# Kernel tuning notes

Measured on AMD Instinct MI355X. Metric: run time of the kernel, lower is better.

The kernel has to match this reference:

```python
import jax, jax.numpy as jnp
import numpy as np


def conv1d(x, w, b):
    # x: (N, Cin, W), w: (Cout, Cin, K) -> (N, Cout, W-K+1), VALID conv (torch Conv1d)
    y = jax.lax.conv_general_dilated(x, w, (1,), 'VALID', dimension_numbers=('NCH', 'OIH', 'NCH'))
    return y + b[None, :, None]


def cnn_block(x, w, b):
    # conv1d then MaxPool1d over the full valid length -> (N, Cout)
    return jnp.max(conv1d(x, w, b), axis=2)


def highway(x, Wp, bp, Wg, bg):
    p = jax.nn.relu(x @ Wp.T + bp)
    g = jax.nn.sigmoid(x @ Wg.T + bg)
    return g * p + (1.0 - g) * x


def lstm_masked(x, lens, Wih, Whh, bih, bhh):
    # x: (N, Wt, E); lens: (N,) valid lengths. Emulates pack_padded_sequence +
    # nn.LSTM + pad_packed_sequence: outputs are h_t for t < len, zeros after.
    N, Wt, _ = x.shape
    H = Whh.shape[1]
    bias = bih + bhh
    h0 = jnp.zeros((N, H), x.dtype)

    def step(carry, inp):
        xt, t = inp
        h, c = carry
        z = xt @ Wih.T + h @ Whh.T + bias  # (N, 4H), gate order i,f,g,o
        i, f, g, o = jnp.split(z, 4, axis=-1)
        c2 = jax.nn.sigmoid(f) * c + jax.nn.sigmoid(i) * jnp.tanh(g)
        h2 = jax.nn.sigmoid(o) * jnp.tanh(c2)
        valid = (t < lens)[:, None]
        h2 = jnp.where(valid, h2, h)
        c2 = jnp.where(valid, c2, c)
        return (h2, c2), jnp.where(valid, h2, jnp.zeros_like(h2))

    xs = jnp.moveaxis(x, 1, 0)  # (Wt, N, E)
    ts = jnp.arange(Wt)
    _, out = jax.lax.scan(step, (h0, h0), (xs, ts))
    return jnp.moveaxis(out, 0, 1)  # (N, Wt, H)


def setup_inputs() -> dict:
    key = jax.random.key(0)
    ks = jax.random.split(key, 32)
    B, T = 32, 48
    WL, WA, WE = 33, 50, 30
    EL, EA, EE, H = 300, 988, 20, 128
    CL, CA, CE = 128, 256, 64
    s = 0.02
    inp = {
        'x_lin': jax.random.normal(ks[0], (B, T, WL, EL), jnp.float32),
        'x_aco': jax.random.normal(ks[1], (B, T, WA, EA), jnp.float32),
        'x_emo': jax.random.normal(ks[2], (B, T, WE, EE), jnp.float32),
        'window_length': jax.random.randint(ks[3], (B, T), 0, WE).astype(jnp.int32) + 1,
        'length': jax.random.randint(ks[4], (B,), 1, T + 1).astype(jnp.int32),
        # CNN params
        'convL_w': s * jax.random.normal(ks[5], (CL, EL, 5), jnp.float32),
        'convL_b': jnp.zeros((CL,), jnp.float32),
        'convA_w': s * jax.random.normal(ks[6], (CA, EA, 10), jnp.float32),
        'convA_b': jnp.zeros((CA,), jnp.float32),
        'convE_w': s * jax.random.normal(ks[7], (CE, H, 3), jnp.float32),
        'convE_b': jnp.zeros((CE,), jnp.float32),
        # Highway params
        'hwL_Wp': s * jax.random.normal(ks[8], (CL, CL), jnp.float32),
        'hwL_bp': jnp.zeros((CL,), jnp.float32),
        'hwL_Wg': s * jax.random.normal(ks[9], (CL, CL), jnp.float32),
        'hwL_bg': jnp.zeros((CL,), jnp.float32),
        'hwA_Wp': s * jax.random.normal(ks[10], (CA, CA), jnp.float32),
        'hwA_bp': jnp.zeros((CA,), jnp.float32),
        'hwA_Wg': s * jax.random.normal(ks[11], (CA, CA), jnp.float32),
        'hwA_bg': jnp.zeros((CA,), jnp.float32),
        'hwE_Wp': s * jax.random.normal(ks[12], (CE, CE), jnp.float32),
        'hwE_bp': jnp.zeros((CE,), jnp.float32),
        'hwE_Wg': s * jax.random.normal(ks[13], (CE, CE), jnp.float32),
        'hwE_bg': jnp.zeros((CE,), jnp.float32),
        # LSTM params (nn.LSTM, 1 layer, batch_first)
        'lstm_Wih': s * jax.random.normal(ks[14], (4 * H, EE), jnp.float32),
        'lstm_Whh': s * jax.random.normal(ks[15], (4 * H, H), jnp.float32),
        'lstm_bih': jnp.zeros((4 * H,), jnp.float32),
        'lstm_bhh': jnp.zeros((4 * H,), jnp.float32),
    }
    return inp


def reference(x_lin, x_aco, x_emo, window_length, length,
              convL_w, convL_b, convA_w, convA_b, convE_w, convE_b,
              hwL_Wp, hwL_bp, hwL_Wg, hwL_bg,
              hwA_Wp, hwA_bp, hwA_Wg, hwA_bg,
              hwE_Wp, hwE_bp, hwE_Wg, hwE_bg,
              lstm_Wih, lstm_Whh, lstm_bih, lstm_bhh):
    B, T = x_lin.shape[:2]
    # Linguistic: per-window CNN + Highway (dropout = identity in eval)
    xl = x_lin.reshape(B * T, x_lin.shape[2], x_lin.shape[3]).transpose(0, 2, 1)  # (BT, 300, WL)
    outL = highway(cnn_block(xl, convL_w, convL_b), hwL_Wp, hwL_bp, hwL_Wg, hwL_bg)
    outL = outL.reshape(B, T, -1)
    # Acoustic
    xa = x_aco.reshape(B * T, x_aco.shape[2], x_aco.shape[3]).transpose(0, 2, 1)  # (BT, 988, WA)
    outA = highway(cnn_block(xa, convA_w, convA_b), hwA_Wp, hwA_bp, hwA_Wg, hwA_bg)
    outA = outA.reshape(B, T, -1)
    # Emotient: ragged per-window LSTM (packed semantics) -> CNN -> Highway
    xe = x_emo.reshape(B * T, x_emo.shape[2], x_emo.shape[3])  # (BT, WE, 20)
    lens = window_length.reshape(B * T)
    h = lstm_masked(xe, lens, lstm_Wih, lstm_Whh, lstm_bih, lstm_bhh)  # (BT, WE, 128)
    outE = highway(cnn_block(h.transpose(0, 2, 1), convE_w, convE_b), hwE_Wp, hwE_bp, hwE_Wg, hwE_bg)
    outE = outE.reshape(B, T, -1)
    # Concatenate modalities -> (B, T, 128+256+64) fed to the downstream head
    return jnp.concatenate([outL, outA, outE], axis=2)
```

## Files before the change

kernel.cpp:

```cpp
#include <hip/hip_runtime.h>
#include <hip/hip_bf16.h>
#include <math.h>

#define BTOT 1536
#define EL 300
#define ELP 304
#define WL_ 33
#define CL 128
#define LOUTL 29
#define KPL 1536
#define EA 988
#define EAP 992
#define WA_ 50
#define CA 256
#define LOUTA 41
#define KPA 9920
#define EE 20
#define WE_ 30
#define HH 128
#define CE 64
#define LOUTE 28
#define KPE 384
#define KDIML 1500
#define KDIMA 9880
#define KDIME 384

typedef __attribute__((ext_vector_type(4))) float f32x4;
typedef __attribute__((ext_vector_type(8))) short short8;

__device__ __forceinline__ unsigned short f2bf(float f) {
    unsigned int x = __float_as_uint(f);
    unsigned int r = (x + 0x7fffu + ((x >> 16) & 1u)) >> 16;
    return (unsigned short)r;
}

__device__ __forceinline__ float sigmf(float x) {
    return __builtin_amdgcn_rcpf(1.f + __expf(-x));
}
__device__ __forceinline__ float tanh_fast(float x) {
    return 1.f - 2.f * __builtin_amdgcn_rcpf(1.f + __expf(2.f * x));
}

#define GLD16(gp, lp) __builtin_amdgcn_global_load_lds( \
    (const __attribute__((address_space(1))) void*)(gp), \
    (__attribute__((address_space(3))) void*)(lp), 16, 0, 0)

template<int N> __device__ __forceinline__ void vmwait() {
    if constexpr (N == 0) asm volatile("s_waitcnt vmcnt(0)" ::: "memory");
    else if constexpr (N == 3) asm volatile("s_waitcnt vmcnt(3)" ::: "memory");
    else if constexpr (N == 4) asm volatile("s_waitcnt vmcnt(4)" ::: "memory");
    else if constexpr (N == 6) asm volatile("s_waitcnt vmcnt(6)" ::: "memory");
    else static_assert(N == 0 || N == 3 || N == 4 || N == 6, "add case");
}

__device__ __forceinline__ void tr_one(const float* a, float* at, int R, int C, int idx) {
    int r = idx / C, c = idx - r * C;
    at[c * R + r] = a[idx];
}
template<int CIN, int CINP, int KW, int COUT, int KPAD>
__device__ __forceinline__ void wt_one(const float* w, unsigned short* wt, int idx) {
    int co = idx / KPAD;
    int p  = idx - co * KPAD;
    int k  = p / CINP;
    int c  = p - k * CINP;
    float v = 0.f;
    if (k < KW && c < CIN) v = w[(co * CIN + c) * KW + k];
    wt[idx] = f2bf(v);
}
template<bool BIG>
__global__ void prep_small(const float* hwL_Wp, float* WpTL, const float* hwL_Wg, float* WgTL,
                           const float* hwA_Wp, float* WpTA, const float* hwA_Wg, float* WgTA,
                           const float* hwE_Wp, float* WpTE, const float* hwE_Wg, float* WgTE,
                           const float* lstm_Wih, float* WihT, const float* lstm_Whh, float* WhhT,
                           const float* convL_w, unsigned short* wtL,
                           const float* convE_w, unsigned short* wtE,
                           unsigned short* whh_bf, unsigned short* wihp_bf) {
    constexpr int S1 = 16384, S2 = 16384, S3 = 65536, S4 = 65536, S5 = 4096, S6 = 4096;
    constexpr int S7 = 512 * 20, S8 = 512 * 128;
    constexpr int S9 = 128 * KPL, S10 = 64 * KPE, S11 = 512 * 128, S12 = 512 * 32;
    constexpr int SMALL = S1 + S2 + S3 + S4 + S5 + S6 + S7 + S8;
    constexpr int TOTAL = BIG ? (SMALL + S9 + S10 + S11 + S12) : SMALL;
    int stride = gridDim.x * blockDim.x;
    for (int i = blockIdx.x * blockDim.x + threadIdx.x; i < TOTAL; i += stride) {
        int idx = i;
        if (idx < S1) { tr_one(hwL_Wp, WpTL, 128, 128, idx); continue; } idx -= S1;
        if (idx < S2) { tr_one(hwL_Wg, WgTL, 128, 128, idx); continue; } idx -= S2;
        if (idx < S3) { tr_one(hwA_Wp, WpTA, 256, 256, idx); continue; } idx -= S3;
        if (idx < S4) { tr_one(hwA_Wg, WgTA, 256, 256, idx); continue; } idx -= S4;
        if (idx < S5) { tr_one(hwE_Wp, WpTE, 64, 64, idx); continue; } idx -= S5;
        if (idx < S6) { tr_one(hwE_Wg, WgTE, 64, 64, idx); continue; } idx -= S6;
        if (idx < S7) { tr_one(lstm_Wih, WihT, 512, 20, idx); continue; } idx -= S7;
        if (idx < S8) { tr_one(lstm_Whh, WhhT, 512, 128, idx); continue; } idx -= S8;
        if constexpr (BIG) {
            if (idx < S9) { wt_one<EL, ELP, 5, CL, KPL>(convL_w, wtL, idx); continue; } idx -= S9;
            if (idx < S10) { wt_one<HH, HH, 3, CE, KPE>(convE_w, wtE, idx); continue; } idx -= S10;
            if (idx < S11) { whh_bf[idx] = f2bf(lstm_Whh[idx]); continue; } idx -= S11;
            { int col = idx >> 5, e = idx & 31;
              wihp_bf[idx] = (e < 20) ? f2bf(lstm_Wih[col * 20 + e]) : (unsigned short)0; }
        }
    }
}

__global__ void prep_wtA(const float* __restrict__ w, unsigned short* __restrict__ wt) {
    int idx = blockIdx.x * blockDim.x + threadIdx.x;
    if (idx >= CA * KPA) return;
    wt_one<EA, EAP, 10, CA, KPA>(w, wt, idx);
}

template<int CIN, int CINP>
__device__ __forceinline__ void cvt_chunk(const float* in, unsigned short* out, int idx) {
    constexpr int CH = CINP / 8;
    int row = idx / CH, c0 = (idx - row * CH) * 8;
    const float* src = in + (size_t)row * CIN + c0;
    union { short8 s; unsigned short u[8]; } o;
    if (c0 + 8 <= CIN) {
        float4 v0 = *(const float4*)src;
        float4 v1 = *(const float4*)(src + 4);
        o.u[0]=f2bf(v0.x); o.u[1]=f2bf(v0.y); o.u[2]=f2bf(v0.z); o.u[3]=f2bf(v0.w);
        o.u[4]=f2bf(v1.x); o.u[5]=f2bf(v1.y); o.u[6]=f2bf(v1.z); o.u[7]=f2bf(v1.w);
    } else {
        #pragma unroll
        for (int j = 0; j < 8; ++j) o.u[j] = (c0 + j < CIN) ? f2bf(src[j]) : (unsigned short)0;
    }
    *(short8*)(out + (size_t)row * CINP + c0) = o.s;
}
__global__ void cvt_both(const float* __restrict__ xa, const float* __restrict__ xl,
                         unsigned short* __restrict__ outa, unsigned short* __restrict__ outl) {
    constexpr int NAC = (BTOT * WA_) * (EAP / 8);
    constexpr int NLC = (BTOT * WL_) * (ELP / 8);
    int stride = gridDim.x * blockDim.x;
    for (int i = blockIdx.x * blockDim.x + threadIdx.x; i < NAC + NLC; i += stride) {
        if (i < NAC) cvt_chunk<EA, EAP>(xa, outa, i);
        else         cvt_chunk<EL, ELP>(xl, outl, i - NAC);
    }
}

template<int NBT, int LOUT, int WIN, int CINP, int COUT, int KPAD, int BM, int BN, int NS>
__global__ __launch_bounds__(256, 2)
void conv_pool_v6(const unsigned short* __restrict__ xb, const unsigned short* __restrict__ wt,
                  const float* __restrict__ bias, float* __restrict__ pooled)
{
    constexpr int MFR  = BM / 32;
    constexpr int NFR  = BN / 32;
    constexpr int A_IT = BM / 64;
    constexpr int B_IT = BN / 64;
    constexpr int VMN  = A_IT + B_IT;
    constexpr int ABY  = BM * 64;
    constexpr int BUFB = (BM + BN) * 64;
    constexpr int NK   = KPAD / 32;
    constexpr int MVAL = NBT * LOUT;
    constexpr int MT   = BTOT / NBT;
    constexpr int EPI  = BM * 36 * 4;
    constexpr int SMSZ = (3 * BUFB > EPI) ? 3 * BUFB : EPI;

    __shared__ __align__(16) char smem[SMSZ];

    const int tid  = threadIdx.x;
    const int lane = tid & 63;
    const int wid  = tid >> 6;
    const int wm   = wid >> 1;
    const int wn   = wid & 1;
    const int lr   = lane & 15;
    const int lq   = lane >> 4;

    int m, n;
    if constexpr (NS == 2) {
        int xcd = blockIdx.x & 7;
        n = xcd & 1;
        m = (xcd >> 1) * (MT / 4) + (blockIdx.x >> 3);
    } else {
        m = blockIdx.x; n = 0;
    }

    f32x4 acc[MFR][NFR];
    #pragma unroll
    for (int i = 0; i < MFR; ++i)
        #pragma unroll
        for (int j = 0; j < NFR; ++j) acc[i][j] = (f32x4){0.f, 0.f, 0.f, 0.f};

    const char* asrc[A_IT];
    #pragma unroll
    for (int i = 0; i < A_IT; ++i) {
        int c = tid + i * 256;
        int r = c >> 2, slot = c & 3;
        int rv = (r < MVAL) ? r : (MVAL - 1);
        int btl = rv / LOUT, l = rv - btl * LOUT;
        asrc[i] = (const char*)xb + (((size_t)(m * NBT + btl) * WIN + l) * CINP) * 2
                + ((slot * 16) ^ (((r >> 1) & 3) << 4));
    }
    const char* bsrc[B_IT];
    #pragma unroll
    for (int i = 0; i < B_IT; ++i) {
        int c = tid + i * 256;
        int col = c >> 2, slot = c & 3;
        bsrc[i] = (const char*)wt + ((size_t)(n * BN + col) * KPAD) * 2
                + ((slot * 16) ^ (((col >> 1) & 3) << 4));
    }

    auto STAGE = [&](int ts, int buf) {
        char* db = smem + buf * BUFB;
        #pragma unroll
        for (int i = 0; i < A_IT; ++i)
            GLD16(asrc[i] + (size_t)ts * 64, db + i * 4096 + wid * 1024);
        #pragma unroll
        for (int i = 0; i < B_IT; ++i)
            GLD16(bsrc[i] + (size_t)ts * 64, db + ABY + i * 4096 + wid * 1024);
    };

    STAGE(0, 0);
    STAGE(1, 1);
    vmwait<VMN>();
    __builtin_amdgcn_s_barrier();

    const int rbase = wm * (BM / 2) + lr;
    const int cbase = wn * (BN / 2) + lr;
    int cur = 0;
    for (int t = 0; t < NK; ++t) {
        const char* sA = smem + cur * BUFB;
        const char* sB = sA + ABY;
        short8 a[MFR];
        #pragma unroll
        for (int o = 0; o < MFR; ++o) {
            int r = rbase + o * 16;
            a[o] = *(const short8*)(sA + (size_t)r * 64 + ((lq * 16) ^ (((r >> 1) & 3) << 4)));
        }
        short8 bfr[NFR];
        #pragma unroll
        for (int nf = 0; nf < NFR; ++nf) {
            int cb = cbase + nf * 16;
            bfr[nf] = *(const short8*)(sB + (size_t)cb * 64 + ((lq * 16) ^ (((cb >> 1) & 3) << 4)));
        }
        int wb = cur + 2; if (wb >= 3) wb -= 3;
        if (t + 2 < NK) STAGE(t + 2, wb);
        asm volatile("s_waitcnt lgkmcnt(0)" ::: "memory");
        __builtin_amdgcn_sched_barrier(0);
        __builtin_amdgcn_s_setprio(1);
        #pragma unroll
        for (int nf = 0; nf < NFR; ++nf)
            #pragma unroll
            for (int o = 0; o < MFR; ++o)
                acc[o][nf] = __builtin_amdgcn_mfma_f32_16x16x32_bf16(a[o], bfr[nf], acc[o][nf], 0, 0, 0);
        __builtin_amdgcn_s_setprio(0);
        if (t + 2 < NK) vmwait<VMN>(); else vmwait<0>();
        asm volatile("" ::: "memory");
        __builtin_amdgcn_s_barrier();
        cur = cur + 1; if (cur >= 3) cur -= 3;
    }
    __syncthreads();

    float* smf = (float*)smem;
    for (int nf = 0; nf < NFR; ++nf) {
        #pragma unroll
        for (int o = 0; o < MFR; ++o) {
            int row = wm * (BM / 2) + o * 16 + lq * 4;
            int cs  = wn * 16 + lr;
            f32x4 v = acc[o][nf];
            #pragma unroll
            for (int r = 0; r < 4; ++r)
                smf[(size_t)(row + r) * 36 + cs] = v[r];
        }
        __syncthreads();
        if (tid < 32 * NBT) {
            int btl = tid >> 5, cs = tid & 31;
            int base = btl * LOUT;
            float mx = smf[(size_t)base * 36 + cs];
            for (int l = 1; l < LOUT; ++l)
                mx = fmaxf(mx, smf[(size_t)(base + l) * 36 + cs]);
            int col = n * BN + (cs >> 4) * (BN / 2) + nf * 16 + (cs & 15);
            int bt  = m * NBT + btl;
            pooled[(size_t)bt * COUT + col] = mx + bias[col];
        }
        __syncthreads();
    }
}

__global__ __launch_bounds__(512, 1)
void lstm_mfma(const float* __restrict__ x_emo,
               const unsigned short* __restrict__ wihp_bf, const unsigned short* __restrict__ whh_bf,
               const float* __restrict__ bih, const float* __restrict__ bhh,
               const int* __restrict__ lens, unsigned short* __restrict__ hbuf)
{
    __shared__ __align__(16) unsigned short xq[WE_ * 16 * 32];
    __shared__ __align__(16) char h_s[2 * 16 * HH * 2];

    const int tid  = threadIdx.x;
    const int w    = tid >> 6;
    const int lane = tid & 63;
    const int lr   = lane & 15;
    const int lq   = lane >> 4;
    const int s0   = blockIdx.x * 16;
    const int c    = w * 16 + lr;

    short8 bfr[4][4];
    short8 bw[4];
    float bj[4];
    #pragma unroll
    for (int g = 0; g < 4; ++g) {
        int col = g * 128 + c;
        #pragma unroll
        for (int kt = 0; kt < 4; ++kt)
            bfr[g][kt] = *(const short8*)(whh_bf + (size_t)col * 128 + kt * 32 + lq * 8);
        bw[g] = *(const short8*)(wihp_bf + (size_t)col * 32 + lq * 8);
        bj[g] = bih[col] + bhh[col];
    }
    int len4[4];
    #pragma unroll
    for (int j = 0; j < 4; ++j) len4[j] = lens[s0 + lq * 4 + j];

    for (int i = tid; i < WE_ * 16 * 32; i += 512) {
        int t = i >> 9, r = (i >> 5) & 15, e = i & 31;
        xq[i] = (e < 20) ? f2bf(x_emo[(((size_t)(s0 + r) * WE_) + t) * 20 + e]) : (unsigned short)0;
    }
    for (int i = tid; i < 2048; i += 512) ((unsigned int*)h_s)[i] = 0u;

    float c_prev[4] = {0.f, 0.f, 0.f, 0.f};
    unsigned short hb_prev[4] = {0, 0, 0, 0};
    __syncthreads();

    for (int t = 0; t < WE_; ++t) {
        const char* hsr = h_s + (t & 1) * 4096;
        char* hsw = h_s + ((t & 1) ^ 1) * 4096;
        short8 ax = *(const short8*)((const char*)xq + (size_t)(t * 16 + lr) * 64 + lq * 16);
        short8 af[4];
        #pragma unroll
        for (int kt = 0; kt < 4; ++kt)
            af[kt] = *(const short8*)(hsr + ((lr * 256 + kt * 64 + lq * 16) ^ ((lr & 7) << 4)));
        f32x4 acc[4];
        #pragma unroll
        for (int g = 0; g < 4; ++g)
            acc[g] = __builtin_amdgcn_mfma_f32_16x16x32_bf16(ax, bw[g], (f32x4){0.f,0.f,0.f,0.f}, 0, 0, 0);
        #pragma unroll
        for (int kt = 0; kt < 4; ++kt)
            #pragma unroll
            for (int g = 0; g < 4; ++g)
                acc[g] = __builtin_amdgcn_mfma_f32_16x16x32_bf16(af[kt], bfr[g][kt], acc[g], 0, 0, 0);
        #pragma unroll
        for (int j = 0; j < 4; ++j) {
            int s = lq * 4 + j;
            float zi = acc[0][j] + bj[0];
            float zf = acc[1][j] + bj[1];
            float zg = acc[2][j] + bj[2];
            float zo = acc[3][j] + bj[3];
            float si = sigmf(zi), sf = sigmf(zf), so = sigmf(zo);
            float tg = tanh_fast(zg);
            float c2 = sf * c_prev[j] + si * tg;
            float h2 = so * tanh_fast(c2);
            bool valid = (t < len4[j]);
            c_prev[j] = valid ? c2 : c_prev[j];
            unsigned short h2b = f2bf(h2);
            unsigned short hn = valid ? h2b : hb_prev[j];
            hb_prev[j] = hn;
            *(unsigned short*)(hsw + (((s * HH + c) * 2) ^ ((s & 7) << 4))) = hn;
            hbuf[(((size_t)(s0 + s) * WE_) + t) * HH + c] = valid ? h2b : (unsigned short)0;
        }
        __syncthreads();
    }
}

__global__ __launch_bounds__(256)
void highway_all(const float* __restrict__ pL, const float* __restrict__ pA, const float* __restrict__ pE,
                 const float* __restrict__ WpTL, const float* __restrict__ bpL,
                 const float* __restrict__ WgTL, const float* __restrict__ bgL,
                 const float* __restrict__ WpTA, const float* __restrict__ bpA,
                 const float* __restrict__ WgTA, const float* __restrict__ bgA,
                 const float* __restrict__ WpTE, const float* __restrict__ bpE,
                 const float* __restrict__ WgTE, const float* __restrict__ bgE,
                 float* __restrict__ out) {
    __shared__ float xs[256];
    int bx = blockIdx.x;
    int tid = threadIdx.x;
    if (bx < BTOT) {
        xs[tid] = pA[(size_t)bx * 256 + tid];
        __syncthreads();
        float ap = bpA[tid], ag = bgA[tid];
        for (int c = 0; c < 256; ++c) {
            float xv = xs[c];
            ap += xv * WpTA[c * 256 + tid];
            ag += xv * WgTA[c * 256 + tid];
        }
        float pp = fmaxf(ap, 0.f);
        float g = sigmf(ag);
        out[(size_t)bx * 448 + 128 + tid] = g * pp + (1.f - g) * xs[tid];
    } else {
        int bt = bx - BTOT;
        if (tid < 128) xs[tid] = pL[(size_t)bt * 128 + tid];
        else if (tid < 192) xs[64 + tid] = pE[(size_t)bt * 64 + (tid - 128)];
        __syncthreads();
        if (tid < 128) {
            float ap = bpL[tid], ag = bgL[tid];
            for (int c = 0; c < 128; ++c) {
                float xv = xs[c];
                ap += xv * WpTL[c * 128 + tid];
                ag += xv * WgTL[c * 128 + tid];
            }
            float pp = fmaxf(ap, 0.f);
            float g = sigmf(ag);
            out[(size_t)bt * 448 + tid] = g * pp + (1.f - g) * xs[tid];
        } else if (tid < 192) {
            int j = tid - 128;
            float ap = bpE[j], ag = bgE[j];
            for (int c = 0; c < 64; ++c) {
                float xv = xs[192 + c];
                ap += xv * WpTE[c * 64 + j];
                ag += xv * WgTE[c * 64 + j];
            }
            float pp = fmaxf(ap, 0.f);
            float g = sigmf(ag);
            out[(size_t)bt * 448 + 384 + j] = g * pp + (1.f - g) * xs[192 + j];
        }
    }
}

__global__ __launch_bounds__(512)
void lstm_kernel_f32(const float* __restrict__ x, const int* __restrict__ lens,
                     const float* __restrict__ WihT, const float* __restrict__ WhhT,
                     const float* __restrict__ bih, const float* __restrict__ bhh,
                     float* __restrict__ hout) {
    int bt = blockIdx.x;
    int j  = threadIdx.x;
    __shared__ float xs[WE_][EE];
    __shared__ __align__(16) float hs[HH];
    __shared__ float zs[512];
    for (int idx = j; idx < WE_ * EE; idx += 512)
        ((float*)xs)[idx] = x[(size_t)bt * WE_ * EE + idx];
    if (j < HH) hs[j] = 0.f;
    float wih[EE];
    #pragma unroll
    for (int e = 0; e < EE; ++e) wih[e] = WihT[e * 512 + j];
    float whh[HH];
    #pragma unroll
    for (int h = 0; h < HH; ++h) whh[h] = WhhT[h * 512 + j];
    float bjv = bih[j] + bhh[j];
    float c_reg = 0.f;
    int len = lens[bt];
    __syncthreads();
    for (int t = 0; t < WE_; ++t) {
        float z = bjv;
        #pragma unroll
        for (int e = 0; e < EE; ++e) z += wih[e] * xs[t][e];
        const float4* h4 = (const float4*)hs;
        #pragma unroll
        for (int q = 0; q < HH / 4; ++q) {
            float4 hv = h4[q];
            z += whh[4*q+0] * hv.x + whh[4*q+1] * hv.y
               + whh[4*q+2] * hv.z + whh[4*q+3] * hv.w;
        }
        zs[j] = z;
        __syncthreads();
        if (j < HH) {
            float zi = zs[j], zf = zs[HH + j], zg = zs[2*HH + j], zo = zs[3*HH + j];
            float si = 1.f / (1.f + expf(-zi));
            float sf = 1.f / (1.f + expf(-zf));
            float so = 1.f / (1.f + expf(-zo));
            float tg = tanhf(zg);
            float c2 = sf * c_reg + si * tg;
            float h2 = so * tanhf(c2);
            bool valid = (t < len);
            float hn = valid ? h2 : hs[j];
            c_reg    = valid ? c2 : c_reg;
            hout[((size_t)bt * WE_ + t) * HH + j] = valid ? h2 : 0.f;
            hs[j] = hn;
        }
        __syncthreads();
    }
}

template<int CIN, int WIN, int COUT, int KDIM, int LOUT>
__global__ __launch_bounds__(256)
void conv_pool_simple(const float* __restrict__ x, const float* __restrict__ w,
                      const float* __restrict__ bias, float* __restrict__ pooled)
{
    constexpr int KW = KDIM / CIN;
    int bt = blockIdx.x;
    int co = blockIdx.y * 64 + (threadIdx.x & 63);
    int seg = threadIdx.x >> 6;
    __shared__ float part[4][64];
    float m = -INFINITY;
    for (int l = seg; l < LOUT; l += 4) {
        float acc = 0.f;
        for (int k = 0; k < KW; ++k) {
            const float* xr = x + ((size_t)bt * WIN + l + k) * CIN;
            const float* wr = w + ((size_t)co * CIN) * KW + k;
            for (int cc = 0; cc < CIN; ++cc) acc += xr[cc] * wr[(size_t)cc * KW];
        }
        m = fmaxf(m, acc);
    }
    part[seg][threadIdx.x & 63] = m;
    __syncthreads();
    if (threadIdx.x < 64) {
        float mm = fmaxf(fmaxf(part[0][threadIdx.x], part[1][threadIdx.x]),
                         fmaxf(part[2][threadIdx.x], part[3][threadIdx.x]));
        pooled[(size_t)bt * COUT + co] = mm + bias[co];
    }
}

static inline int cdiv(int a, int b) { return (a + b - 1) / b; }

extern "C" void kernel_launch(void* const* d_in, const int* in_sizes, int n_in,
                              void* d_out, int out_size, void* d_ws, size_t ws_size,
                              hipStream_t stream) {
    const float* x_lin  = (const float*)d_in[0];
    const float* x_aco  = (const float*)d_in[1];
    const float* x_emo  = (const float*)d_in[2];
    const int*   wlen   = (const int*)  d_in[3];
    const float* convL_w = (const float*)d_in[5];
    const float* convL_b = (const float*)d_in[6];
    const float* convA_w = (const float*)d_in[7];
    const float* convA_b = (const float*)d_in[8];
    const float* convE_w = (const float*)d_in[9];
    const float* convE_b = (const float*)d_in[10];
    const float* hwL_Wp = (const float*)d_in[11];
    const float* hwL_bp = (const float*)d_in[12];
    const float* hwL_Wg = (const float*)d_in[13];
    const float* hwL_bg = (const float*)d_in[14];
    const float* hwA_Wp = (const float*)d_in[15];
    const float* hwA_bp = (const float*)d_in[16];
    const float* hwA_Wg = (const float*)d_in[17];
    const float* hwA_bg = (const float*)d_in[18];
    const float* hwE_Wp = (const float*)d_in[19];
    const float* hwE_bp = (const float*)d_in[20];
    const float* hwE_Wg = (const float*)d_in[21];
    const float* hwE_bg = (const float*)d_in[22];
    const float* lstm_Wih = (const float*)d_in[23];
    const float* lstm_Whh = (const float*)d_in[24];
    const float* lstm_bih = (const float*)d_in[25];
    const float* lstm_bhh = (const float*)d_in[26];
    float* out = (float*)d_out;

    char* p0 = (char*)d_ws;
    char* p = p0;
    auto alloc = [&](size_t bytes) { char* r = p; p += (bytes + 255) & ~(size_t)255; return r; };
    float* WpTL = (float*)alloc((size_t)CL * CL * 4);
    float* WgTL = (float*)alloc((size_t)CL * CL * 4);
    float* WpTA = (float*)alloc((size_t)CA * CA * 4);
    float* WgTA = (float*)alloc((size_t)CA * CA * 4);
    float* WpTE = (float*)alloc((size_t)CE * CE * 4);
    float* WgTE = (float*)alloc((size_t)CE * CE * 4);
    float* WihT = (float*)alloc((size_t)EE * 512 * 4);
    float* WhhT = (float*)alloc((size_t)HH * 512 * 4);
    unsigned short* whh_bf  = (unsigned short*)alloc((size_t)512 * 128 * 2);
    unsigned short* wihp_bf = (unsigned short*)alloc((size_t)512 * 32 * 2);
    void*  hbuf = (void*)alloc((size_t)BTOT * WE_ * HH * 4);
    float* pL   = (float*)alloc((size_t)BTOT * CL * 4);
    float* pA   = (float*)alloc((size_t)BTOT * CA * 4);
    float* pE   = (float*)alloc((size_t)BTOT * CE * 4);
    unsigned short* wtA = (unsigned short*)alloc((size_t)CA * KPA * 2);
    unsigned short* wtL = (unsigned short*)alloc((size_t)CL * KPL * 2);
    unsigned short* wtE = (unsigned short*)alloc((size_t)CE * KPE * 2);
    unsigned short* xlin_p = (unsigned short*)alloc((size_t)BTOT * WL_ * ELP * 2 + 64);
    unsigned short* xaco_p = (unsigned short*)alloc((size_t)BTOT * WA_ * EAP * 2 + 64);
    size_t need = (size_t)(p - p0);
    bool big = ws_size >= need;

    if (big) {
        prep_small<true><<<2048, 256, 0, stream>>>(hwL_Wp, WpTL, hwL_Wg, WgTL, hwA_Wp, WpTA, hwA_Wg, WgTA,
                                                   hwE_Wp, WpTE, hwE_Wg, WgTE, lstm_Wih, WihT, lstm_Whh, WhhT,
                                                   convL_w, wtL, convE_w, wtE, whh_bf, wihp_bf);
        prep_wtA<<<cdiv(CA * KPA, 256), 256, 0, stream>>>(convA_w, wtA);
        lstm_mfma<<<BTOT / 16, 512, 0, stream>>>(x_emo, wihp_bf, whh_bf, lstm_bih, lstm_bhh, wlen,
                                                 (unsigned short*)hbuf);
        cvt_both<<<4096, 256, 0, stream>>>(x_aco, x_lin, xaco_p, xlin_p);
        conv_pool_v6<6, LOUTA, WA_, EAP, CA, KPA, 256, 128, 2>
            <<<512, 256, 0, stream>>>(xaco_p, wtA, convA_b, pA);
        conv_pool_v6<4, LOUTL, WL_, ELP, CL, KPL, 128, 128, 1>
            <<<BTOT / 4, 256, 0, stream>>>(xlin_p, wtL, convL_b, pL);
        conv_pool_v6<4, LOUTE, WE_, HH, CE, KPE, 128, 64, 1>
            <<<BTOT / 4, 256, 0, stream>>>((const unsigned short*)hbuf, wtE, convE_b, pE);
    } else {
        prep_small<false><<<2048, 256, 0, stream>>>(hwL_Wp, WpTL, hwL_Wg, WgTL, hwA_Wp, WpTA, hwA_Wg, WgTA,
                                                    hwE_Wp, WpTE, hwE_Wg, WgTE, lstm_Wih, WihT, lstm_Whh, WhhT,
                                                    convL_w, wtL, convE_w, wtE, whh_bf, wihp_bf);
        lstm_kernel_f32<<<BTOT, 512, 0, stream>>>(x_emo, wlen, WihT, WhhT, lstm_bih, lstm_bhh, (float*)hbuf);
        conv_pool_simple<EA, WA_, CA, KDIMA, LOUTA>
            <<<dim3(BTOT, CA / 64), 256, 0, stream>>>(x_aco, convA_w, convA_b, pA);
        conv_pool_simple<EL, WL_, CL, KDIML, LOUTL>
            <<<dim3(BTOT, CL / 64), 256, 0, stream>>>(x_lin, convL_w, convL_b, pL);
        conv_pool_simple<HH, WE_, CE, KDIME, LOUTE>
            <<<dim3(BTOT, CE / 64), 256, 0, stream>>>((const float*)hbuf, convE_w, convE_b, pE);
    }

    highway_all<<<2 * BTOT, 256, 0, stream>>>(pL, pA, pE,
                                              WpTL, hwL_bp, WgTL, hwL_bg,
                                              WpTA, hwA_bp, WgTA, hwA_bg,
                                              WpTE, hwE_bp, WgTE, hwE_bg, out);
}
```

Baseline: 627.4 us.

## Rewrite conv-pool as shifted-window implicit GEMM and fuse prep/cvt launches

Replaces the im2col-style conv_pool_v6 with conv_pool_v8, which loads each input window chunk once into LDS and reuses it across all kernel taps by shifting rows. It also pools in registers with lane shuffles instead of an LDS epilogue. The weight layout changes to per-tap channel blocks, so ELP is padded to 320 for 32-aligned chunks. The conv A weight prep moves into the shared prep kernel, and the input bf16 conversion runs as extra blocks of the LSTM kernel, cutting launches and overlapping the conversion with the serial LSTM. This adds wasted padded K work for the linguistic path and uses hand-tuned vmcnt waits that must match the issue order exactly.

```diff
diff --git a/kernel.cpp b/kernel.cpp
--- a/kernel.cpp
+++ b/kernel.cpp
@@ -4,11 +4,11 @@
 
 #define BTOT 1536
 #define EL 300
-#define ELP 304
+#define ELP 320
 #define WL_ 33
 #define CL 128
 #define LOUTL 29
-#define KPL 1536
+#define KPL 1600
 #define EA 988
 #define EAP 992
 #define WA_ 50
@@ -47,10 +47,13 @@
 
 template<int N> __device__ __forceinline__ void vmwait() {
     if constexpr (N == 0) asm volatile("s_waitcnt vmcnt(0)" ::: "memory");
-    else if constexpr (N == 3) asm volatile("s_waitcnt vmcnt(3)" ::: "memory");
+    else if constexpr (N == 1) asm volatile("s_waitcnt vmcnt(1)" ::: "memory");
+    else if constexpr (N == 2) asm volatile("s_waitcnt vmcnt(2)" ::: "memory");
     else if constexpr (N == 4) asm volatile("s_waitcnt vmcnt(4)" ::: "memory");
+    else if constexpr (N == 5) asm volatile("s_waitcnt vmcnt(5)" ::: "memory");
     else if constexpr (N == 6) asm volatile("s_waitcnt vmcnt(6)" ::: "memory");
-    else static_assert(N == 0 || N == 3 || N == 4 || N == 6, "add case");
+    else if constexpr (N == 8) asm volatile("s_waitcnt vmcnt(8)" ::: "memory");
+    else static_assert(N == 0, "add case");
 }
 
 __device__ __forceinline__ void tr_one(const float* a, float* at, int R, int C, int idx) {
@@ -68,18 +71,20 @@
     wt[idx] = f2bf(v);
 }
 template<bool BIG>
-__global__ void prep_small(const float* hwL_Wp, float* WpTL, const float* hwL_Wg, float* WgTL,
-                           const float* hwA_Wp, float* WpTA, const float* hwA_Wg, float* WgTA,
-                           const float* hwE_Wp, float* WpTE, const float* hwE_Wg, float* WgTE,
-                           const float* lstm_Wih, float* WihT, const float* lstm_Whh, float* WhhT,
-                           const float* convL_w, unsigned short* wtL,
-                           const float* convE_w, unsigned short* wtE,
-                           unsigned short* whh_bf, unsigned short* wihp_bf) {
+__global__ void prep_all(const float* hwL_Wp, float* WpTL, const float* hwL_Wg, float* WgTL,
+                         const float* hwA_Wp, float* WpTA, const float* hwA_Wg, float* WgTA,
+                         const float* hwE_Wp, float* WpTE, const float* hwE_Wg, float* WgTE,
+                         const float* lstm_Wih, float* WihT, const float* lstm_Whh, float* WhhT,
+                         const float* convL_w, unsigned short* wtL,
+                         const float* convE_w, unsigned short* wtE,
+                         const float* convA_w, unsigned short* wtA,
+                         unsigned short* whh_bf, unsigned short* wihp_bf) {
     constexpr int S1 = 16384, S2 = 16384, S3 = 65536, S4 = 65536, S5 = 4096, S6 = 4096;
     constexpr int S7 = 512 * 20, S8 = 512 * 128;
     constexpr int S9 = 128 * KPL, S10 = 64 * KPE, S11 = 512 * 128, S12 = 512 * 32;
+    constexpr int S13 = CA * KPA;
     constexpr int SMALL = S1 + S2 + S3 + S4 + S5 + S6 + S7 + S8;
-    constexpr int TOTAL = BIG ? (SMALL + S9 + S10 + S11 + S12) : SMALL;
+    constexpr int TOTAL = BIG ? (SMALL + S9 + S10 + S11 + S12 + S13) : SMALL;
     int stride = gridDim.x * blockDim.x;
     for (int i = blockIdx.x * blockDim.x + threadIdx.x; i < TOTAL; i += stride) {
         int idx = i;
@@ -95,16 +100,12 @@
             if (idx < S9) { wt_one<EL, ELP, 5, CL, KPL>(convL_w, wtL, idx); continue; } idx -= S9;
             if (idx < S10) { wt_one<HH, HH, 3, CE, KPE>(convE_w, wtE, idx); continue; } idx -= S10;
             if (idx < S11) { whh_bf[idx] = f2bf(lstm_Whh[idx]); continue; } idx -= S11;
-            { int col = idx >> 5, e = idx & 31;
-              wihp_bf[idx] = (e < 20) ? f2bf(lstm_Wih[col * 20 + e]) : (unsigned short)0; }
-        }
-    }
-}
-
-__global__ void prep_wtA(const float* __restrict__ w, unsigned short* __restrict__ wt) {
-    int idx = blockIdx.x * blockDim.x + threadIdx.x;
-    if (idx >= CA * KPA) return;
-    wt_one<EA, EAP, 10, CA, KPA>(w, wt, idx);
+            if (idx < S12) { int col = idx >> 5, e = idx & 31;
+                             wihp_bf[idx] = (e < 20) ? f2bf(lstm_Wih[col * 20 + e]) : (unsigned short)0;
+                             continue; } idx -= S12;
+            wt_one<EA, EAP, 10, CA, KPA>(convA_w, wtA, idx);
+        }
+    }
 }
 
 template<int CIN, int CINP>
@@ -124,164 +125,31 @@
     }
     *(short8*)(out + (size_t)row * CINP + c0) = o.s;
 }
-__global__ void cvt_both(const float* __restrict__ xa, const float* __restrict__ xl,
-                         unsigned short* __restrict__ outa, unsigned short* __restrict__ outl) {
-    constexpr int NAC = (BTOT * WA_) * (EAP / 8);
-    constexpr int NLC = (BTOT * WL_) * (ELP / 8);
-    int stride = gridDim.x * blockDim.x;
-    for (int i = blockIdx.x * blockDim.x + threadIdx.x; i < NAC + NLC; i += stride) {
-        if (i < NAC) cvt_chunk<EA, EAP>(xa, outa, i);
-        else         cvt_chunk<EL, ELP>(xl, outl, i - NAC);
-    }
-}
-
-template<int NBT, int LOUT, int WIN, int CINP, int COUT, int KPAD, int BM, int BN, int NS>
-__global__ __launch_bounds__(256, 2)
-void conv_pool_v6(const unsigned short* __restrict__ xb, const unsigned short* __restrict__ wt,
-                  const float* __restrict__ bias, float* __restrict__ pooled)
-{
-    constexpr int MFR  = BM / 32;
-    constexpr int NFR  = BN / 32;
-    constexpr int A_IT = BM / 64;
-    constexpr int B_IT = BN / 64;
-    constexpr int VMN  = A_IT + B_IT;
-    constexpr int ABY  = BM * 64;
-    constexpr int BUFB = (BM + BN) * 64;
-    constexpr int NK   = KPAD / 32;
-    constexpr int MVAL = NBT * LOUT;
-    constexpr int MT   = BTOT / NBT;
-    constexpr int EPI  = BM * 36 * 4;
-    constexpr int SMSZ = (3 * BUFB > EPI) ? 3 * BUFB : EPI;
-
-    __shared__ __align__(16) char smem[SMSZ];
-
-    const int tid  = threadIdx.x;
-    const int lane = tid & 63;
-    const int wid  = tid >> 6;
-    const int wm   = wid >> 1;
-    const int wn   = wid & 1;
-    const int lr   = lane & 15;
-    const int lq   = lane >> 4;
-
-    int m, n;
-    if constexpr (NS == 2) {
-        int xcd = blockIdx.x & 7;
-        n = xcd & 1;
-        m = (xcd >> 1) * (MT / 4) + (blockIdx.x >> 3);
-    } else {
-        m = blockIdx.x; n = 0;
-    }
-
-    f32x4 acc[MFR][NFR];
-    #pragma unroll
-    for (int i = 0; i < MFR; ++i)
-        #pragma unroll
-        for (int j = 0; j < NFR; ++j) acc[i][j] = (f32x4){0.f, 0.f, 0.f, 0.f};
-
-    const char* asrc[A_IT];
-    #pragma unroll
-    for (int i = 0; i < A_IT; ++i) {
-        int c = tid + i * 256;
-        int r = c >> 2, slot = c & 3;
-        int rv = (r < MVAL) ? r : (MVAL - 1);
-        int btl = rv / LOUT, l = rv - btl * LOUT;
-        asrc[i] = (const char*)xb + (((size_t)(m * NBT + btl) * WIN + l) * CINP) * 2
-                + ((slot * 16) ^ (((r >> 1) & 3) << 4));
-    }
-    const char* bsrc[B_IT];
-    #pragma unroll
-    for (int i = 0; i < B_IT; ++i) {
-        int c = tid + i * 256;
-        int col = c >> 2, slot = c & 3;
-        bsrc[i] = (const char*)wt + ((size_t)(n * BN + col) * KPAD) * 2
-                + ((slot * 16) ^ (((col >> 1) & 3) << 4));
-    }
-
-    auto STAGE = [&](int ts, int buf) {
-        char* db = smem + buf * BUFB;
-        #pragma unroll
-        for (int i = 0; i < A_IT; ++i)
-            GLD16(asrc[i] + (size_t)ts * 64, db + i * 4096 + wid * 1024);
-        #pragma unroll
-        for (int i = 0; i < B_IT; ++i)
-            GLD16(bsrc[i] + (size_t)ts * 64, db + ABY + i * 4096 + wid * 1024);
-    };
-
-    STAGE(0, 0);
-    STAGE(1, 1);
-    vmwait<VMN>();
-    __builtin_amdgcn_s_barrier();
-
-    const int rbase = wm * (BM / 2) + lr;
-    const int cbase = wn * (BN / 2) + lr;
-    int cur = 0;
-    for (int t = 0; t < NK; ++t) {
-        const char* sA = smem + cur * BUFB;
-        const char* sB = sA + ABY;
-        short8 a[MFR];
-        #pragma unroll
-        for (int o = 0; o < MFR; ++o) {
-            int r = rbase + o * 16;
-            a[o] = *(const short8*)(sA + (size_t)r * 64 + ((lq * 16) ^ (((r >> 1) & 3) << 4)));
-        }
-        short8 bfr[NFR];
-        #pragma unroll
-        for (int nf = 0; nf < NFR; ++nf) {
-            int cb = cbase + nf * 16;
-            bfr[nf] = *(const short8*)(sB + (size_t)cb * 64 + ((lq * 16) ^ (((cb >> 1) & 3) << 4)));
-        }
-        int wb = cur + 2; if (wb >= 3) wb -= 3;
-        if (t + 2 < NK) STAGE(t + 2, wb);
-        asm volatile("s_waitcnt lgkmcnt(0)" ::: "memory");
-        __builtin_amdgcn_sched_barrier(0);
-        __builtin_amdgcn_s_setprio(1);
-        #pragma unroll
-        for (int nf = 0; nf < NFR; ++nf)
-            #pragma unroll
-            for (int o = 0; o < MFR; ++o)
-                acc[o][nf] = __builtin_amdgcn_mfma_f32_16x16x32_bf16(a[o], bfr[nf], acc[o][nf], 0, 0, 0);
-        __builtin_amdgcn_s_setprio(0);
-        if (t + 2 < NK) vmwait<VMN>(); else vmwait<0>();
-        asm volatile("" ::: "memory");
-        __builtin_amdgcn_s_barrier();
-        cur = cur + 1; if (cur >= 3) cur -= 3;
-    }
-    __syncthreads();
-
-    float* smf = (float*)smem;
-    for (int nf = 0; nf < NFR; ++nf) {
-        #pragma unroll
-        for (int o = 0; o < MFR; ++o) {
-            int row = wm * (BM / 2) + o * 16 + lq * 4;
-            int cs  = wn * 16 + lr;
-            f32x4 v = acc[o][nf];
-            #pragma unroll
-            for (int r = 0; r < 4; ++r)
-                smf[(size_t)(row + r) * 36 + cs] = v[r];
-        }
-        __syncthreads();
-        if (tid < 32 * NBT) {
-            int btl = tid >> 5, cs = tid & 31;
-            int base = btl * LOUT;
-            float mx = smf[(size_t)base * 36 + cs];
-            for (int l = 1; l < LOUT; ++l)
-                mx = fmaxf(mx, smf[(size_t)(base + l) * 36 + cs]);
-            int col = n * BN + (cs >> 4) * (BN / 2) + nf * 16 + (cs & 15);
-            int bt  = m * NBT + btl;
-            pooled[(size_t)bt * COUT + col] = mx + bias[col];
-        }
-        __syncthreads();
-    }
-}
+
+#define LSTM_BLOCKS 96
+#define CVT_BLOCKS 1952
 
 __global__ __launch_bounds__(512, 1)
-void lstm_mfma(const float* __restrict__ x_emo,
-               const unsigned short* __restrict__ wihp_bf, const unsigned short* __restrict__ whh_bf,
-               const float* __restrict__ bih, const float* __restrict__ bhh,
-               const int* __restrict__ lens, unsigned short* __restrict__ hbuf)
+void lstm_cvt(const float* __restrict__ x_emo,
+              const unsigned short* __restrict__ wihp_bf, const unsigned short* __restrict__ whh_bf,
+              const float* __restrict__ bih, const float* __restrict__ bhh,
+              const int* __restrict__ lens, unsigned short* __restrict__ hbuf,
+              const float* __restrict__ xa, const float* __restrict__ xl,
+              unsigned short* __restrict__ outa, unsigned short* __restrict__ outl)
 {
     __shared__ __align__(16) unsigned short xq[WE_ * 16 * 32];
     __shared__ __align__(16) char h_s[2 * 16 * HH * 2];
+
+    if (blockIdx.x >= LSTM_BLOCKS) {
+        constexpr int NAC = (BTOT * WA_) * (EAP / 8);
+        constexpr int NLC = (BTOT * WL_) * (ELP / 8);
+        int stride = CVT_BLOCKS * 512;
+        for (int i = (blockIdx.x - LSTM_BLOCKS) * 512 + threadIdx.x; i < NAC + NLC; i += stride) {
+            if (i < NAC) cvt_chunk<EA, EAP>(xa, outa, i);
+            else         cvt_chunk<EL, ELP>(xl, outl, i - NAC);
+        }
+        return;
+    }
 
     const int tid  = threadIdx.x;
     const int w    = tid >> 6;
@@ -354,6 +222,179 @@
             hbuf[(((size_t)(s0 + s) * WE_) + t) * HH + c] = valid ? h2b : (unsigned short)0;
         }
         __syncthreads();
+    }
+}
+
+template<int LOUT, int WIN, int CINP, int KW, int BN, int NS, int MFR, int COUT>
+__global__ __launch_bounds__(256, 2)
+void conv_pool_v8(const unsigned short* __restrict__ xb, const unsigned short* __restrict__ wt,
+                  const float* __restrict__ bias, float* __restrict__ pooled)
+{
+    constexpr int CCH   = CINP / 32;
+    constexpr int KB    = CINP * 2;
+    constexpr int KTOTB = CINP * KW * 2;
+    constexpr int NFR   = BN / 16;
+    constexpr int B_IT  = BN / 64;
+    constexpr int ABUF  = 4 * 64 * 64;
+    constexpr int BBUF  = BN * 64;
+    constexpr int CPQ   = (BTOT / 4) / 4;
+
+    __shared__ __align__(16) char smem[2 * ABUF + 4 * BBUF];
+
+    const int tid  = threadIdx.x;
+    const int lane = tid & 63;
+    const int wid  = tid >> 6;
+    const int lr   = lane & 15;
+    const int lq   = lane >> 4;
+    const int lq16 = lq * 16;
+
+    int m, n;
+    if constexpr (NS == 2) {
+        int xcd = blockIdx.x & 7;
+        n = xcd & 1;
+        m = (xcd >> 1) * CPQ + (blockIdx.x >> 3);
+    } else {
+        m = blockIdx.x; n = 0;
+    }
+
+    f32x4 acc[MFR][NFR];
+    #pragma unroll
+    for (int i = 0; i < MFR; ++i)
+        #pragma unroll
+        for (int j = 0; j < NFR; ++j) acc[i][j] = (f32x4){0.f, 0.f, 0.f, 0.f};
+
+    const int aw_r = tid >> 2;
+    const int aw   = (aw_r < WIN) ? aw_r : (WIN - 1);
+    const int slot = tid & 3;
+    const char* asrc[4];
+    #pragma unroll
+    for (int i = 0; i < 4; ++i)
+        asrc[i] = (const char*)xb + ((size_t)((m * 4 + i) * WIN + aw)) * KB
+                + ((slot * 16) ^ (((aw_r >> 1) & 3) << 4));
+    const char* bsrc[B_IT];
+    #pragma unroll
+    for (int i = 0; i < B_IT; ++i) {
+        int col = (tid + i * 256) >> 2;
+        bsrc[i] = (const char*)wt + (size_t)(n * BN + col) * KTOTB
+                + ((slot * 16) ^ (((col >> 1) & 3) << 4));
+    }
+
+    char* const abuf0 = smem;
+    char* const abuf1 = smem + ABUF;
+    char* const bbase = smem + 2 * ABUF;
+
+    int cbo[NFR];
+    #pragma unroll
+    for (int nf = 0; nf < NFR; ++nf) {
+        int cb = nf * 16 + lr;
+        cbo[nf] = cb * 64 + (lq16 ^ (((cb >> 1) & 3) << 4));
+    }
+
+    #pragma unroll
+    for (int i = 0; i < 4; ++i)
+        GLD16(asrc[i], abuf0 + i * 4096 + tid * 16);
+    #pragma unroll
+    for (int s = 0; s < 3; ++s)
+        #pragma unroll
+        for (int i = 0; i < B_IT; ++i)
+            GLD16(bsrc[i] + s * KB, bbase + s * BBUF + i * 4096 + tid * 16);
+    vmwait<0>();
+    __builtin_amdgcn_s_barrier();
+
+    int bcur = 0;
+
+#define STEP(KK, WN, TAIL) do {                                                    \
+    const char* bb = bbase + bcur * BBUF;                                          \
+    short8 afr[MFR];                                                               \
+    _Pragma("unroll")                                                              \
+    for (int o = 0; o < MFR; ++o) {                                                \
+        int row = o * 16 + lr + (KK);                                              \
+        afr[o] = *(const short8*)(awave + row * 64 + (lq16 ^ (((row >> 1) & 3) << 4))); \
+    }                                                                              \
+    short8 bf[NFR];                                                                \
+    _Pragma("unroll")                                                              \
+    for (int nf = 0; nf < NFR; ++nf) bf[nf] = *(const short8*)(bb + cbo[nf]);      \
+    if (!(TAIL) || (KK) < KW - 3) {                                                \
+        constexpr int k3_ = ((KK) + 3 < KW) ? (KK) + 3 : (KK) + 3 - KW;            \
+        int boff = k3_ * KB + (((KK) + 3 < KW) ? ci : ci + 1) * 64;                \
+        char* bstg = bbase + ((bcur + 3) & 3) * BBUF;                              \
+        _Pragma("unroll")                                                          \
+        for (int i = 0; i < B_IT; ++i)                                             \
+            GLD16(bsrc[i] + boff, bstg + i * 4096 + tid * 16);                     \
+    }                                                                              \
+    if (!(TAIL)) {                                                                 \
+        if (KW >= 8) {                                                             \
+            if ((KK) < 4)                                                          \
+                GLD16(asrc[(KK) & 3] + (size_t)(ci + 1) * 64, abn + ((KK) & 3) * 4096 + tid * 16); \
+        } else if ((KK) == 0) {                                                    \
+            _Pragma("unroll")                                                      \
+            for (int i = 0; i < 4; ++i)                                            \
+                GLD16(asrc[i] + (size_t)(ci + 1) * 64, abn + i * 4096 + tid * 16); \
+        }                                                                          \
+    }                                                                              \
+    asm volatile("s_waitcnt lgkmcnt(0)" ::: "memory");                             \
+    __builtin_amdgcn_sched_barrier(0);                                             \
+    __builtin_amdgcn_s_setprio(1);                                                 \
+    _Pragma("unroll")                                                              \
+    for (int nf = 0; nf < NFR; ++nf)                                               \
+        _Pragma("unroll")                                                          \
+        for (int o = 0; o < MFR; ++o)                                              \
+            acc[o][nf] = __builtin_amdgcn_mfma_f32_16x16x32_bf16(afr[o], bf[nf], acc[o][nf], 0, 0, 0); \
+    __builtin_amdgcn_s_setprio(0);                                                 \
+    vmwait<WN>();                                                                  \
+    asm volatile("" ::: "memory");                                                 \
+    __builtin_amdgcn_s_barrier();                                                  \
+    bcur = (bcur + 1) & 3;                                                         \
+} while (0)
+
+    for (int ci = 0; ci < CCH - 1; ++ci) {
+        const char* ab = (ci & 1) ? abuf1 : abuf0;
+        char* abn = (ci & 1) ? abuf0 : abuf1;
+        const char* awave = ab + wid * 4096;
+        if constexpr (KW == 10) {
+            STEP(0, 5, false); STEP(1, 6, false); STEP(2, 6, false); STEP(3, 6, false);
+            STEP(4, 5, false); STEP(5, 4, false); STEP(6, 4, false); STEP(7, 4, false);
+            STEP(8, 4, false); STEP(9, 4, false);
+        } else if constexpr (KW == 5) {
+            STEP(0, 8, false); STEP(1, 8, false); STEP(2, 4, false); STEP(3, 4, false); STEP(4, 4, false);
+        } else {
+            STEP(0, 6, false); STEP(1, 6, false); STEP(2, 2, false);
+        }
+    }
+    {
+        const int ci = CCH - 1;
+        const char* ab = (ci & 1) ? abuf1 : abuf0;
+        char* abn = (ci & 1) ? abuf0 : abuf1; (void)abn;
+        const char* awave = ab + wid * 4096;
+        if constexpr (KW == 10) {
+            STEP(0, 4, true); STEP(1, 4, true); STEP(2, 4, true); STEP(3, 4, true);
+            STEP(4, 4, true); STEP(5, 4, true); STEP(6, 4, true); STEP(7, 2, true);
+            STEP(8, 0, true); STEP(9, 0, true);
+        } else if constexpr (KW == 5) {
+            STEP(0, 4, true); STEP(1, 4, true); STEP(2, 2, true); STEP(3, 0, true); STEP(4, 0, true);
+        } else {
+            STEP(0, 1, true); STEP(1, 0, true); STEP(2, 0, true);
+        }
+    }
+#undef STEP
+
+    const int bt = m * 4 + wid;
+    #pragma unroll
+    for (int nf = 0; nf < NFR; ++nf) {
+        float mx = -INFINITY;
+        #pragma unroll
+        for (int o = 0; o < MFR; ++o) {
+            int rb = o * 16 + lq * 4;
+            #pragma unroll
+            for (int j = 0; j < 4; ++j)
+                if (rb + j < LOUT) mx = fmaxf(mx, acc[o][nf][j]);
+        }
+        mx = fmaxf(mx, __shfl_xor(mx, 16, 64));
+        mx = fmaxf(mx, __shfl_xor(mx, 32, 64));
+        if (lane < 16) {
+            int col = n * BN + nf * 16 + lane;
+            pooled[(size_t)bt * COUT + col] = mx + bias[col];
+        }
     }
 }
 
@@ -553,23 +594,22 @@
     bool big = ws_size >= need;
 
     if (big) {
-        prep_small<true><<<2048, 256, 0, stream>>>(hwL_Wp, WpTL, hwL_Wg, WgTL, hwA_Wp, WpTA, hwA_Wg, WgTA,
-                                                   hwE_Wp, WpTE, hwE_Wg, WgTE, lstm_Wih, WihT, lstm_Whh, WhhT,
-                                                   convL_w, wtL, convE_w, wtE, whh_bf, wihp_bf);
-        prep_wtA<<<cdiv(CA * KPA, 256), 256, 0, stream>>>(convA_w, wtA);
-        lstm_mfma<<<BTOT / 16, 512, 0, stream>>>(x_emo, wihp_bf, whh_bf, lstm_bih, lstm_bhh, wlen,
-                                                 (unsigned short*)hbuf);
-        cvt_both<<<4096, 256, 0, stream>>>(x_aco, x_lin, xaco_p, xlin_p);
-        conv_pool_v6<6, LOUTA, WA_, EAP, CA, KPA, 256, 128, 2>
-            <<<512, 256, 0, stream>>>(xaco_p, wtA, convA_b, pA);
-        conv_pool_v6<4, LOUTL, WL_, ELP, CL, KPL, 128, 128, 1>
-            <<<BTOT / 4, 256, 0, stream>>>(xlin_p, wtL, convL_b, pL);
-        conv_pool_v6<4, LOUTE, WE_, HH, CE, KPE, 128, 64, 1>
-            <<<BTOT / 4, 256, 0, stream>>>((const unsigned short*)hbuf, wtE, convE_b, pE);
+        prep_all<true><<<2048, 256, 0, stream>>>(hwL_Wp, WpTL, hwL_Wg, WgTL, hwA_Wp, WpTA, hwA_Wg, WgTA,
+                                                 hwE_Wp, WpTE, hwE_Wg, WgTE, lstm_Wih, WihT, lstm_Whh, WhhT,
+                                                 convL_w, wtL, convE_w, wtE, convA_w, wtA, whh_bf, wihp_bf);
+        lstm_cvt<<<LSTM_BLOCKS + CVT_BLOCKS, 512, 0, stream>>>(
+            x_emo, wihp_bf, whh_bf, lstm_bih, lstm_bhh, wlen, (unsigned short*)hbuf,
+            x_aco, x_lin, xaco_p, xlin_p);
+        conv_pool_v8<LOUTA, WA_, EAP, 10, 128, 2, 3, CA>
+            <<<768, 256, 0, stream>>>(xaco_p, wtA, convA_b, pA);
+        conv_pool_v8<LOUTL, WL_, ELP, 5, 128, 1, 2, CL>
+            <<<384, 256, 0, stream>>>(xlin_p, wtL, convL_b, pL);
+        conv_pool_v8<LOUTE, WE_, HH, 3, 64, 1, 2, CE>
+            <<<384, 256, 0, stream>>>((const unsigned short*)hbuf, wtE, convE_b, pE);
     } else {
-        prep_small<false><<<2048, 256, 0, stream>>>(hwL_Wp, WpTL, hwL_Wg, WgTL, hwA_Wp, WpTA, hwA_Wg, WgTA,
-                                                    hwE_Wp, WpTE, hwE_Wg, WgTE, lstm_Wih, WihT, lstm_Whh, WhhT,
-                                                    convL_w, wtL, convE_w, wtE, whh_bf, wihp_bf);
+        prep_all<false><<<2048, 256, 0, stream>>>(hwL_Wp, WpTL, hwL_Wg, WgTL, hwA_Wp, WpTA, hwA_Wg, WgTA,
+                                                  hwE_Wp, WpTE, hwE_Wg, WgTE, lstm_Wih, WihT, lstm_Whh, WhhT,
+                                                  convL_w, wtL, convE_w, wtE, convA_w, wtA, whh_bf, wihp_bf);
         lstm_kernel_f32<<<BTOT, 512, 0, stream>>>(x_emo, wlen, WihT, WhhT, lstm_bih, lstm_bhh, (float*)hbuf);
         conv_pool_simple<EA, WA_, CA, KDIMA, LOUTA>
             <<<dim3(BTOT, CA / 64), 256, 0, stream>>>(x_aco, convA_w, convA_b, pA);
```

After: 567.9 us. 1.1x faster.
